# Kernel tuning notes

Hardware: AMD Instinct MI355X
Metric: run time of the kernel (lower is better)

The kernel has to match this reference:

```python
import jax, jax.numpy as jnp
import numpy as np

DIM_MODEL = 1024
N_HEAD = 16
N_HEAD_H = 16
DIM_KEY = 64
DIM_VALUE = 64


def _linear_params(key, out_f, in_f):
    kw, kb = jax.random.split(key)
    bound = 1.0 / np.sqrt(in_f)
    W = jax.random.uniform(kw, (out_f, in_f), jnp.float32, -bound, bound)
    b = jax.random.uniform(kb, (out_f,), jnp.float32, -bound, bound)
    return W, b


def setup_inputs() -> dict:
    key = jax.random.key(0)
    ks = jax.random.split(key, 12)
    B, L = 4, 1024
    queries = jax.random.normal(ks[0], (B, L, DIM_MODEL), jnp.float32)
    keys = jax.random.normal(ks[1], (B, L, DIM_MODEL), jnp.float32)
    values = jax.random.normal(ks[2], (B, L, DIM_MODEL), jnp.float32)
    mask = jnp.ones((B, L), dtype=jnp.bool_)  # accepted but unused by the module
    attn_bias = jax.random.normal(ks[3], (B, N_HEAD, L), jnp.float32)
    Wq, bq = _linear_params(ks[4], DIM_KEY * N_HEAD, DIM_MODEL)
    Wk, bk = _linear_params(ks[5], DIM_KEY * N_HEAD, DIM_MODEL)
    Wv, bv = _linear_params(ks[6], DIM_VALUE * N_HEAD, DIM_MODEL)
    Wl, bl = _linear_params(ks[7], N_HEAD_H, N_HEAD)
    Ww, bw = _linear_params(ks[8], N_HEAD, N_HEAD_H)
    Wo, bo = _linear_params(ks[9], DIM_MODEL, DIM_VALUE * N_HEAD)
    return {
        "queries": queries, "keys": keys, "values": values,
        "mask": mask, "attn_bias": attn_bias,
        "Wq": Wq, "bq": bq, "Wk": Wk, "bk": bk, "Wv": Wv, "bv": bv,
        "Wl": Wl, "bl": bl, "Ww": Ww, "bw": bw, "Wo": Wo, "bo": bo,
    }


def reference(queries, keys, values, mask, attn_bias,
              Wq, bq, Wk, bk, Wv, bv, Wl, bl, Ww, bw, Wo, bo):
    B, Lq, _ = queries.shape
    # projections -> [B, L, H, d]
    q = (queries @ Wq.T + bq).reshape(B, Lq, N_HEAD, DIM_KEY)
    k = (keys @ Wk.T + bk).reshape(B, keys.shape[1], N_HEAD, DIM_KEY)
    v = (values @ Wv.T + bv).reshape(B, values.shape[1], N_HEAD, DIM_VALUE)
    scale = DIM_KEY ** (-0.5)
    # scores in the module's [B, Lq, Lk, H] layout (after its two transposes)
    scores = jnp.einsum("bqhd,bkhd->bqkh", scale * q, k)
    # attn_bias [B, H, Lq] -> [B, Lq, 1, H], broadcast over Lk
    scores = scores + jnp.transpose(attn_bias, (0, 2, 1))[:, :, None, :]
    # pre-softmax head mixing (fc_l): [B, Lq, Lk, H] -> [B, Lq, Lk, Hh]
    logits = jnp.einsum("bqkh,gh->bqkg", scores, Wl) + bl
    weights = jax.nn.softmax(logits, axis=2)  # softmax over Lk
    # post-softmax head mixing (fc_w): [B, Lq, Lk, Hh] -> [B, Lq, Lk, H]
    weights = jnp.einsum("bqkg,hg->bqkh", weights, Ww) + bw
    # weighted values: [B, Lq, H, dv] -> combine heads -> fc_o
    ctx = jnp.einsum("bqkh,bkhd->bqhd", weights, v).reshape(B, Lq, N_HEAD * DIM_VALUE)
    return ctx @ Wo.T + bo
```

## Files before the change

### kernel.cpp

```cpp
#include <hip/hip_runtime.h>

#define L_ 1024
#define DM 1024

typedef float f32x4 __attribute__((ext_vector_type(4)));
typedef _Float16 f16;
typedef _Float16 f16x8 __attribute__((ext_vector_type(8)));
typedef _Float16 f16x4 __attribute__((ext_vector_type(4)));

__device__ __forceinline__ void gload16(const void* g, void* l) {
  __builtin_amdgcn_global_load_lds(
      (const __attribute__((address_space(1))) unsigned int*)g,
      (__attribute__((address_space(3))) unsigned int*)l, 16, 0, 0);
}

__global__ __launch_bounds__(256) void cvt_all(const float* __restrict__ q,
    const float* __restrict__ k, const float* __restrict__ v,
    const float* __restrict__ wq, const float* __restrict__ wk,
    const float* __restrict__ wv, const float* __restrict__ wo,
    f16* __restrict__ dbig, f16* __restrict__ dw, f16* __restrict__ dwo) {
  int i = blockIdx.x * 256 + threadIdx.x;
  const float* s; f16* d; int off;
  if (i < 524288)       { s = q;  d = dbig;           off = i; }
  else if (i < 1048576) { s = k;  d = dbig + 4194304; off = i - 524288; }
  else if (i < 1572864) { s = v;  d = dbig + 8388608; off = i - 1048576; }
  else if (i < 1703936) { s = wq; d = dw;             off = i - 1572864; }
  else if (i < 1835008) { s = wk; d = dw + 1048576;   off = i - 1703936; }
  else if (i < 1966080) { s = wv; d = dw + 2097152;   off = i - 1835008; }
  else                  { s = wo; d = dwo;            off = i - 1966080; }
  const float4* sp = (const float4*)s + (size_t)off * 2;
  float4 a = sp[0], bb = sp[1];
  f16x8 o;
  o[0] = (f16)a.x;  o[1] = (f16)a.y;  o[2] = (f16)a.z;  o[3] = (f16)a.w;
  o[4] = (f16)bb.x; o[5] = (f16)bb.y; o[6] = (f16)bb.z; o[7] = (f16)bb.w;
  ((f16x8*)d)[off] = o;
}

__global__ __launch_bounds__(256) void biascat(const float* __restrict__ bq,
    const float* __restrict__ bk, const float* __restrict__ bv, float* __restrict__ o) {
  int t = blockIdx.x * 256 + threadIdx.x;
  o[t] = (t < 1024) ? bq[t] : (t < 2048) ? bk[t - 1024] : bv[t - 2048];
}

__global__ __launch_bounds__(256) void proj_gemm(const f16* __restrict__ Ain,
    const f16* __restrict__ Wc, const float* __restrict__ bcat, f16* __restrict__ QKVp) {
  alignas(16) __shared__ f16 At[128 * 32];
  alignas(16) __shared__ f16 Bt[128 * 32];
  int z = blockIdx.z;
  const f16* A = Ain + (size_t)z * 4194304;
  const f16* W = Wc + (size_t)z * 1048576;
  int t = threadIdx.x, lane = t & 63;
  int w = t >> 6, wr = w >> 1, wc = w & 1;
  int bm = blockIdx.y * 128, bn = blockIdx.x * 128;
  f32x4 acc[4][4] = {};
  int rb = 32 * w + (lane >> 2);
  int c8 = (lane & 3) * 8;
  const f16* gA = A + (size_t)(bm + rb) * 1024 + c8;
  const f16* gB = W + (size_t)(bn + rb) * 1024 + c8;
  f16* lA0 = &At[(2 * w) * 512];
  f16* lA1 = &At[(2 * w + 1) * 512];
  f16* lB0 = &Bt[(2 * w) * 512];
  f16* lB1 = &Bt[(2 * w + 1) * 512];
  int ro = (lane & 15) * 32 + (lane >> 4) * 8;
  for (int kk = 0; kk < 1024; kk += 32) {
    gload16(gA + kk, lA0);
    gload16(gA + 16 * 1024 + kk, lA1);
    gload16(gB + kk, lB0);
    gload16(gB + 16 * 1024 + kk, lB1);
    __syncthreads();
    f16x8 af[4], bf[4];
    #pragma unroll
    for (int m = 0; m < 4; ++m) af[m] = *(const f16x8*)&At[(wr * 64 + m * 16) * 32 + ro];
    #pragma unroll
    for (int n = 0; n < 4; ++n) bf[n] = *(const f16x8*)&Bt[(wc * 64 + n * 16) * 32 + ro];
    #pragma unroll
    for (int m = 0; m < 4; ++m)
      #pragma unroll
      for (int n = 0; n < 4; ++n)
        acc[m][n] = __builtin_amdgcn_mfma_f32_16x16x32_f16(af[m], bf[n], acc[m][n], 0, 0, 0);
    __syncthreads();
  }
  float scale = (z == 0) ? 0.125f : 1.0f;
  #pragma unroll
  for (int n = 0; n < 4; ++n) {
    int cn = bn + wc * 64 + n * 16 + (lane & 15);
    float bvv = bcat[z * 1024 + cn];
    #pragma unroll
    for (int m = 0; m < 4; ++m) {
      int r0 = bm + wr * 64 + m * 16 + (lane >> 4) * 4;
      #pragma unroll
      for (int r = 0; r < 4; ++r)
        QKVp[(size_t)(r0 + r) * 3072 + z * 1024 + cn] = (f16)((acc[m][n][r] + bvv) * scale);
    }
  }
}

__global__ __launch_bounds__(256) void gemm_out(const f16* __restrict__ A,
    const f16* __restrict__ W, const float* __restrict__ bias, float* __restrict__ C) {
  alignas(16) __shared__ f16 At[128 * 32];
  alignas(16) __shared__ f16 Bt[128 * 32];
  int t = threadIdx.x, lane = t & 63;
  int w = t >> 6, wr = w >> 1, wc = w & 1;
  int bm = blockIdx.y * 128, bn = blockIdx.x * 128;
  f32x4 acc[4][4] = {};
  int rb = 32 * w + (lane >> 2);
  int c8 = (lane & 3) * 8;
  const f16* gA = A + (size_t)(bm + rb) * 1024 + c8;
  const f16* gB = W + (size_t)(bn + rb) * 1024 + c8;
  f16* lA0 = &At[(2 * w) * 512];
  f16* lA1 = &At[(2 * w + 1) * 512];
  f16* lB0 = &Bt[(2 * w) * 512];
  f16* lB1 = &Bt[(2 * w + 1) * 512];
  int ro = (lane & 15) * 32 + (lane >> 4) * 8;
  for (int kk = 0; kk < 1024; kk += 32) {
    gload16(gA + kk, lA0);
    gload16(gA + 16 * 1024 + kk, lA1);
    gload16(gB + kk, lB0);
    gload16(gB + 16 * 1024 + kk, lB1);
    __syncthreads();
    f16x8 af[4], bf[4];
    #pragma unroll
    for (int m = 0; m < 4; ++m) af[m] = *(const f16x8*)&At[(wr * 64 + m * 16) * 32 + ro];
    #pragma unroll
    for (int n = 0; n < 4; ++n) bf[n] = *(const f16x8*)&Bt[(wc * 64 + n * 16) * 32 + ro];
    #pragma unroll
    for (int m = 0; m < 4; ++m)
      #pragma unroll
      for (int n = 0; n < 4; ++n)
        acc[m][n] = __builtin_amdgcn_mfma_f32_16x16x32_f16(af[m], bf[n], acc[m][n], 0, 0, 0);
    __syncthreads();
  }
  #pragma unroll
  for (int n = 0; n < 4; ++n) {
    int cn = bn + wc * 64 + n * 16 + (lane & 15);
    float bvv = bias[cn];
    #pragma unroll
    for (int m = 0; m < 4; ++m) {
      int r0 = bm + wr * 64 + m * 16 + (lane >> 4) * 4;
      #pragma unroll
      for (int r = 0; r < 4; ++r)
        C[(size_t)(r0 + r) * 1024 + cn] = acc[m][n][r] + bvv;
    }
  }
}

__global__ __launch_bounds__(256) void transpose_v(const f16* __restrict__ QKVp,
                                                   f16* __restrict__ Vt) {
  alignas(16) __shared__ f16 T[64 * 72];
  int bh = blockIdx.y;
  int b = bh >> 4, h = bh & 15;
  int kt = blockIdx.x;
  int t = threadIdx.x;
  int krow = t >> 2, part = t & 3;
  const f16x8* src = (const f16x8*)(QKVp + (size_t)(b * L_ + kt * 64 + krow) * 3072 + 2048 + h * 64 + part * 16);
  f16x8 v0 = src[0], v1 = src[1];
  *(f16x8*)&T[krow * 72 + part * 16] = v0;
  *(f16x8*)&T[krow * 72 + part * 16 + 8] = v1;
  __syncthreads();
  int drow = t >> 2;
  f16x8 o0, o1;
  #pragma unroll
  for (int j = 0; j < 8; ++j) o0[j] = T[(part * 16 + j) * 72 + drow];
  #pragma unroll
  for (int j = 0; j < 8; ++j) o1[j] = T[(part * 16 + 8 + j) * 72 + drow];
  f16* dst = Vt + (size_t)(bh * 64 + drow) * L_ + kt * 64 + part * 16;
  *(f16x8*)dst = o0;
  *(f16x8*)(dst + 8) = o1;
}

__global__ __launch_bounds__(256) void cbias_kernel(const float* __restrict__ ab,
    const float* __restrict__ Wl, const float* __restrict__ bl, float* __restrict__ cb) {
  int t = blockIdx.x * 256 + threadIdx.x;
  int b = t >> 14, q = (t >> 4) & 1023, g = t & 15;
  float s = bl[g];
  #pragma unroll
  for (int h = 0; h < 16; ++h) s += ab[(size_t)(b * 16 + h) * L_ + q] * Wl[g * 16 + h];
  cb[t] = s;
}

__global__ __launch_bounds__(256) void qk_gemm(const f16* __restrict__ QKVp,
                                               f16* __restrict__ S, int b0) {
  alignas(16) __shared__ f16 At[128 * 72];
  alignas(16) __shared__ f16 Bt[128 * 72];
  int t = threadIdx.x, lane = t & 63;
  int wid = t >> 6, wr = wid >> 1, wc = wid & 1;
  int kt = blockIdx.x, qt = blockIdx.y;
  int h = blockIdx.z & 15, bz = blockIdx.z >> 4;
  int b = b0 + bz;
  #pragma unroll
  for (int i = 0; i < 4; ++i) {
    int row = i * 32 + (t >> 3), c = (t & 7) * 8;
    *(f16x8*)&At[row * 72 + c] =
        *(const f16x8*)(QKVp + (size_t)(b * 1024 + qt * 128 + row) * 3072 + h * 64 + c);
    *(f16x8*)&Bt[row * 72 + c] =
        *(const f16x8*)(QKVp + (size_t)(b * 1024 + kt * 128 + row) * 3072 + 1024 + h * 64 + c);
  }
  __syncthreads();
  int l15 = lane & 15, lhi = lane >> 4;
  f32x4 acc[4][4] = {};
  #pragma unroll
  for (int s = 0; s < 2; ++s) {
    f16x8 af[4], bf[4];
    #pragma unroll
    for (int m = 0; m < 4; ++m) af[m] = *(const f16x8*)&At[(wr * 64 + m * 16 + l15) * 72 + s * 32 + lhi * 8];
    #pragma unroll
    for (int n = 0; n < 4; ++n) bf[n] = *(const f16x8*)&Bt[(wc * 64 + n * 16 + l15) * 72 + s * 32 + lhi * 8];
    #pragma unroll
    for (int m = 0; m < 4; ++m)
      #pragma unroll
      for (int n = 0; n < 4; ++n)
        acc[m][n] = __builtin_amdgcn_mfma_f32_16x16x32_f16(af[m], bf[n], acc[m][n], 0, 0, 0);
  }
  size_t Sh = (size_t)(bz * 16 + h) * 1048576;
  #pragma unroll
  for (int n = 0; n < 4; ++n) {
    int col = kt * 128 + wc * 64 + n * 16 + l15;
    #pragma unroll
    for (int m = 0; m < 4; ++m) {
      int q0 = qt * 128 + wr * 64 + m * 16 + lhi * 4;
      #pragma unroll
      for (int r = 0; r < 4; ++r)
        S[Sh + (size_t)(q0 + r) * 1024 + col] = (f16)acc[m][n][r];
    }
  }
}

__global__ __launch_bounds__(256, 1) void msm_kernel(f16* __restrict__ S,
    const float* __restrict__ Wl, const float* __restrict__ Ww,
    const float* __restrict__ bwv, const float* __restrict__ cb, int b0) {
  alignas(16) __shared__ f16 Sl[16][1032];
  alignas(16) __shared__ f16 Sl2[1024][18];
  __shared__ float red[4][16];
  __shared__ float rlv16[16];
  int t = threadIdx.x;
  int q = blockIdx.x & 1023, bz = blockIdx.x >> 10;
  int lane = t & 63, w = t >> 6, l15 = lane & 15, lhi = lane >> 4;
  size_t Sq = (size_t)(bz * 16) * 1048576 + (size_t)q * 1024;
  #pragma unroll
  for (int i = 0; i < 8; ++i) {
    int idx = i * 256 + t, h = idx >> 7, c = (idx & 127) * 8;
    *(f16x8*)&Sl[h][c] = *(const f16x8*)(S + Sq + (size_t)h * 1048576 + c);
  }
  f16x4 b1;
  #pragma unroll
  for (int j = 0; j < 4; ++j) b1[j] = (f16)Wl[l15 * 16 + lhi * 4 + j];
  float cbv = cb[((size_t)((b0 + bz) * 1024 + q)) * 16 + l15];
  __syncthreads();
  float dsum = 0.f;
  for (int i = 0; i < 16; ++i) {
    int kt = w * 16 + i;
    int krow = kt * 16 + l15;
    f16x4 a1;
    #pragma unroll
    for (int j = 0; j < 4; ++j) a1[j] = Sl[lhi * 4 + j][krow];
    f32x4 d = __builtin_amdgcn_mfma_f32_16x16x16f16(a1, b1, (f32x4){0.f, 0.f, 0.f, 0.f}, 0, 0, 0);
    int k0 = kt * 16 + lhi * 4;
    #pragma unroll
    for (int r = 0; r < 4; ++r) {
      float e = __expf(d[r] + cbv);
      dsum += e;
      Sl2[k0 + r][l15] = (f16)e;
    }
  }
  dsum += __shfl_xor(dsum, 16);
  dsum += __shfl_xor(dsum, 32);
  if (lane < 16) red[w][lane] = dsum;
  __syncthreads();
  if (t < 16) rlv16[t] = 1.0f / (red[0][t] + red[1][t] + red[2][t] + red[3][t]);
  __syncthreads();
  f16x4 b2;
  #pragma unroll
  for (int j = 0; j < 4; ++j) b2[j] = (f16)(Ww[l15 * 16 + lhi * 4 + j] * rlv16[lhi * 4 + j]);
  float bwh = bwv[l15];
  for (int i = 0; i < 16; ++i) {
    int kt = w * 16 + i;
    int krow = kt * 16 + l15;
    f16x4 a2;
    #pragma unroll
    for (int j = 0; j < 4; ++j) a2[j] = Sl2[krow][lhi * 4 + j];
    f32x4 d = __builtin_amdgcn_mfma_f32_16x16x16f16(a2, b2, (f32x4){0.f, 0.f, 0.f, 0.f}, 0, 0, 0);
    int k0 = kt * 16 + lhi * 4;
    #pragma unroll
    for (int r = 0; r < 4; ++r) Sl[l15][k0 + r] = (f16)(d[r] + bwh);
  }
  __syncthreads();
  #pragma unroll
  for (int i = 0; i < 8; ++i) {
    int idx = i * 256 + t, h = idx >> 7, c = (idx & 127) * 8;
    *(f16x8*)(S + Sq + (size_t)h * 1048576 + c) = *(f16x8*)&Sl[h][c];
  }
}

__global__ __launch_bounds__(256) void pv_gemm(const f16* __restrict__ Sw,
    const f16* __restrict__ Vt, f16* __restrict__ ctx, int b0) {
  alignas(16) __shared__ f16 Aw[32 * 72];
  alignas(16) __shared__ f16 Bv[64 * 72];
  int t = threadIdx.x, lane = t & 63, w = t >> 6;
  int qt = blockIdx.x, h = blockIdx.y, bz = blockIdx.z;
  int wr = w >> 1, wc = w & 1;
  int l15 = lane & 15, lhi = lane >> 4;
  const f16* Sh = Sw + (size_t)(bz * 16 + h) * 1048576 + (size_t)(qt * 32) * 1024;
  const f16* Vh = Vt + (size_t)((b0 + bz) * 16 + h) * 64 * 1024;
  f32x4 acc[2] = {};
  int srow = t >> 3, scol = (t & 7) * 8;
  for (int kk = 0; kk < 1024; kk += 64) {
    __syncthreads();
    *(f16x8*)&Aw[srow * 72 + scol] = *(const f16x8*)(Sh + (size_t)srow * 1024 + kk + scol);
    *(f16x8*)&Bv[srow * 72 + scol] = *(const f16x8*)(Vh + (size_t)srow * 1024 + kk + scol);
    *(f16x8*)&Bv[(srow + 32) * 72 + scol] = *(const f16x8*)(Vh + (size_t)(srow + 32) * 1024 + kk + scol);
    __syncthreads();
    #pragma unroll
    for (int s = 0; s < 2; ++s) {
      f16x8 af = *(const f16x8*)&Aw[(wr * 16 + l15) * 72 + s * 32 + lhi * 8];
      #pragma unroll
      for (int n = 0; n < 2; ++n) {
        f16x8 bf = *(const f16x8*)&Bv[(wc * 32 + n * 16 + l15) * 72 + s * 32 + lhi * 8];
        acc[n] = __builtin_amdgcn_mfma_f32_16x16x32_f16(af, bf, acc[n], 0, 0, 0);
      }
    }
  }
  #pragma unroll
  for (int n = 0; n < 2; ++n) {
    int col = h * 64 + wc * 32 + n * 16 + l15;
    int q0 = (b0 + bz) * 1024 + qt * 32 + wr * 16 + lhi * 4;
    #pragma unroll
    for (int r = 0; r < 4; ++r)
      ctx[(size_t)(q0 + r) * 1024 + col] = (f16)acc[n][r];
  }
}

extern "C" void kernel_launch(void* const* d_in, const int* in_sizes, int n_in,
                              void* d_out, int out_size, void* d_ws, size_t ws_size,
                              hipStream_t stream) {
  const float* queries = (const float*)d_in[0];
  const float* keys    = (const float*)d_in[1];
  const float* values  = (const float*)d_in[2];
  const float* ab  = (const float*)d_in[4];
  const float* Wq  = (const float*)d_in[5];  const float* bq = (const float*)d_in[6];
  const float* Wk  = (const float*)d_in[7];  const float* bk = (const float*)d_in[8];
  const float* Wv  = (const float*)d_in[9];  const float* bv = (const float*)d_in[10];
  const float* Wl  = (const float*)d_in[11]; const float* bl = (const float*)d_in[12];
  const float* Ww  = (const float*)d_in[13]; const float* bwp = (const float*)d_in[14];
  const float* Wo  = (const float*)d_in[15]; const float* bo = (const float*)d_in[16];

  char* ws = (char*)d_ws;
  const size_t MB = 1024 * 1024;
  bool full = ws_size >= 172 * MB;

  f16* qin   = (f16*)(ws + 0 * MB);
  f16* wqkv  = (f16*)(ws + 24 * MB);
  f16* S     = (f16*)(ws + 0 * MB);
  f16* QKVp  = (f16*)(ws + (full ? 128 : 32) * MB);
  f16* Vt    = (f16*)(ws + (full ? 152 : 56) * MB);
  float* cbp = (float*)(ws + (full ? 170 : 64) * MB);
  f16* wo16  = (f16*)(ws + (full ? 168 : 65) * MB);
  f16* ctx   = (f16*)(ws + (full ? 160 : 67) * MB);
  float* bqkv = (float*)(ws + (full ? 170 * MB + 512 * 1024 : 30 * MB));

  cvt_all<<<8192, 256, 0, stream>>>(queries, keys, values, Wq, Wk, Wv, Wo, qin, wqkv, wo16);
  biascat<<<12, 256, 0, stream>>>(bq, bk, bv, bqkv);
  proj_gemm<<<dim3(8, 32, 3), 256, 0, stream>>>(qin, wqkv, bqkv, QKVp);
  transpose_v<<<dim3(16, 64), 256, 0, stream>>>(QKVp, Vt);
  cbias_kernel<<<256, 256, 0, stream>>>(ab, Wl, bl, cbp);

  if (full) {
    qk_gemm<<<dim3(8, 8, 64), 256, 0, stream>>>(QKVp, S, 0);
    msm_kernel<<<4096, 256, 0, stream>>>(S, Wl, Ww, bwp, cbp, 0);
    pv_gemm<<<dim3(32, 16, 4), 256, 0, stream>>>(S, Vt, ctx, 0);
  } else {
    for (int b = 0; b < 4; ++b) {
      qk_gemm<<<dim3(8, 8, 16), 256, 0, stream>>>(QKVp, S, b);
      msm_kernel<<<1024, 256, 0, stream>>>(S, Wl, Ww, bwp, cbp, b);
      pv_gemm<<<dim3(32, 16, 1), 256, 0, stream>>>(S, Vt, ctx, b);
    }
  }

  gemm_out<<<dim3(8, 32), 256, 0, stream>>>(ctx, wo16, bo, (float*)d_out);
}
```

Measured before the change: 213.7 us.

## Fuse QK scores with head-mixing softmax via two-pass recompute, dropping scores buffer

Replaces the separate qk_gemm and msm_kernel with a fused attn_ab kernel that computes QK scores in registers and applies the pre-softmax head mix with packed fp16 dot2. A first pass accumulates the softmax denominators per key quarter, combine_rl reduces them, and a second pass recomputes the scores, normalises, applies the post-softmax mix and writes only the final weights. This removes the write and read-back of the raw score tensor, at the cost of computing QK twice and launching only 256 blocks with heavy register use. It also drops the low-workspace fallback path and assumes the large workspace is always available.

```diff
diff --git a/kernel.cpp b/kernel.cpp
--- a/kernel.cpp
+++ b/kernel.cpp
@@ -7,12 +7,29 @@
 typedef _Float16 f16;
 typedef _Float16 f16x8 __attribute__((ext_vector_type(8)));
 typedef _Float16 f16x4 __attribute__((ext_vector_type(4)));
+typedef _Float16 f16x2 __attribute__((ext_vector_type(2)));
 
 __device__ __forceinline__ void gload16(const void* g, void* l) {
   __builtin_amdgcn_global_load_lds(
       (const __attribute__((address_space(1))) unsigned int*)g,
       (__attribute__((address_space(3))) unsigned int*)l, 16, 0, 0);
 }
+
+__device__ __forceinline__ f16x2 pkrtz(float a, float b) {
+  return __builtin_bit_cast(f16x2, __builtin_amdgcn_cvt_pkrtz(a, b));
+}
+
+#if __has_builtin(__builtin_amdgcn_fdot2)
+__device__ __forceinline__ float DOT2(f16x2 a, f16x2 b, float c) {
+  return __builtin_amdgcn_fdot2(__builtin_bit_cast(__fp16 __attribute__((ext_vector_type(2))), a),
+                                __builtin_bit_cast(__fp16 __attribute__((ext_vector_type(2))), b),
+                                c, false);
+}
+#else
+__device__ __forceinline__ float DOT2(f16x2 a, f16x2 b, float c) {
+  return fmaf((float)a[0], (float)b[0], fmaf((float)a[1], (float)b[1], c));
+}
+#endif
 
 __global__ __launch_bounds__(256) void cvt_all(const float* __restrict__ q,
     const float* __restrict__ k, const float* __restrict__ v,
@@ -178,117 +195,194 @@
   cb[t] = s;
 }
 
-__global__ __launch_bounds__(256) void qk_gemm(const f16* __restrict__ QKVp,
-                                               f16* __restrict__ S, int b0) {
-  alignas(16) __shared__ f16 At[128 * 72];
-  alignas(16) __shared__ f16 Bt[128 * 72];
-  int t = threadIdx.x, lane = t & 63;
-  int wid = t >> 6, wr = wid >> 1, wc = wid & 1;
-  int kt = blockIdx.x, qt = blockIdx.y;
-  int h = blockIdx.z & 15, bz = blockIdx.z >> 4;
-  int b = b0 + bz;
-  #pragma unroll
-  for (int i = 0; i < 4; ++i) {
-    int row = i * 32 + (t >> 3), c = (t & 7) * 8;
-    *(f16x8*)&At[row * 72 + c] =
-        *(const f16x8*)(QKVp + (size_t)(b * 1024 + qt * 128 + row) * 3072 + h * 64 + c);
-    *(f16x8*)&Bt[row * 72 + c] =
-        *(const f16x8*)(QKVp + (size_t)(b * 1024 + kt * 128 + row) * 3072 + 1024 + h * 64 + c);
-  }
-  __syncthreads();
+template <int WRITE_W>
+__global__ __launch_bounds__(256, 1) void attn_ab(const f16* __restrict__ QKVp,
+    const float* __restrict__ Wl, const float* __restrict__ Ww, const float* __restrict__ bwv,
+    const float* __restrict__ cbp, const float* __restrict__ rlp,
+    float* __restrict__ denomP, f16* __restrict__ wG) {
+  alignas(16) __shared__ f16 Kl[2][16][1032];
+  __shared__ f16x2 wlp[16][8];
+  int bid = blockIdx.x;
+  int x = bid & 7, y = bid >> 3;
+  int b = x >> 1, qt = y & 15, kq = ((x & 1) << 1) | (y >> 4);
+  int t = threadIdx.x, lane = t & 63, wv = t >> 6;
   int l15 = lane & 15, lhi = lane >> 4;
-  f32x4 acc[4][4] = {};
-  #pragma unroll
-  for (int s = 0; s < 2; ++s) {
-    f16x8 af[4], bf[4];
-    #pragma unroll
-    for (int m = 0; m < 4; ++m) af[m] = *(const f16x8*)&At[(wr * 64 + m * 16 + l15) * 72 + s * 32 + lhi * 8];
-    #pragma unroll
-    for (int n = 0; n < 4; ++n) bf[n] = *(const f16x8*)&Bt[(wc * 64 + n * 16 + l15) * 72 + s * 32 + lhi * 8];
-    #pragma unroll
-    for (int m = 0; m < 4; ++m)
-      #pragma unroll
-      for (int n = 0; n < 4; ++n)
-        acc[m][n] = __builtin_amdgcn_mfma_f32_16x16x32_f16(af[m], bf[n], acc[m][n], 0, 0, 0);
-  }
-  size_t Sh = (size_t)(bz * 16 + h) * 1048576;
-  #pragma unroll
-  for (int n = 0; n < 4; ++n) {
-    int col = kt * 128 + wc * 64 + n * 16 + l15;
-    #pragma unroll
-    for (int m = 0; m < 4; ++m) {
-      int q0 = qt * 128 + wr * 64 + m * 16 + lhi * 4;
+  if (t < 128) {
+    int g = t >> 3, p = t & 7;
+    wlp[g][p] = pkrtz(Wl[g * 16 + 2 * p], Wl[g * 16 + 2 * p + 1]);
+  }
+  int qg = b * 1024 + qt * 64 + wv * 16 + l15;
+  f16x8 qf[16][2];
+  #pragma unroll
+  for (int h = 0; h < 16; ++h)
+    #pragma unroll
+    for (int s = 0; s < 2; ++s)
+      qf[h][s] = *(const f16x8*)(QKVp + (size_t)qg * 3072 + h * 64 + s * 32 + lhi * 8);
+  float cbl[16];
+  #pragma unroll
+  for (int g4 = 0; g4 < 4; ++g4)
+    *(f32x4*)&cbl[g4 * 4] = *(const f32x4*)(cbp + (size_t)qg * 16 + g4 * 4);
+  float rlv[16];
+  float dacc[16] = {};
+  if constexpr (WRITE_W) {
+    #pragma unroll
+    for (int g4 = 0; g4 < 4; ++g4)
+      *(f32x4*)&rlv[g4 * 4] = *(const f32x4*)(rlp + (size_t)qg * 16 + g4 * 4);
+  }
+
+  auto stage = [&](int nb, int it) {
+    int k0 = b * 1024 + kq * 256 + it * 16;
+    #pragma unroll
+    for (int j = 0; j < 4; ++j) {
+      int row = wv * 4 + j;
+      const f16* src = QKVp + (size_t)(k0 + row) * 3072 + 1024 + lane * 8;
+      gload16(src, &Kl[nb][row][0]);
+      gload16(src + 512, &Kl[nb][row][512]);
+    }
+  };
+
+  if constexpr (WRITE_W) {
+    __shared__ f16x2 wwp[16][8];
+    alignas(16) __shared__ f16 WT[16][64][20];
+    if (t >= 128) {
+      int h = (t - 128) >> 3, p = (t - 128) & 7;
+      wwp[h][p] = pkrtz(Ww[h * 16 + 2 * p], Ww[h * 16 + 2 * p + 1]);
+    }
+    float bwl[16];
+    #pragma unroll
+    for (int h = 0; h < 16; ++h) bwl[h] = bwv[h];
+    stage(0, 0);
+    __syncthreads();
+    for (int it = 0; it < 16; ++it) {
+      int cur = it & 1;
+      if (it < 15) stage(cur ^ 1, it + 1);
+      f32x4 acc[16];
+      #pragma unroll
+      for (int h = 0; h < 16; ++h) {
+        f16x8 a0 = *(const f16x8*)&Kl[cur][l15][h * 64 + lhi * 8];
+        f16x8 a1 = *(const f16x8*)&Kl[cur][l15][h * 64 + 32 + lhi * 8];
+        acc[h] = __builtin_amdgcn_mfma_f32_16x16x32_f16(a0, qf[h][0], (f32x4){0.f, 0.f, 0.f, 0.f}, 0, 0, 0);
+        acc[h] = __builtin_amdgcn_mfma_f32_16x16x32_f16(a1, qf[h][1], acc[h], 0, 0, 0);
+      }
+      f16x2 sp[4][8];
+      #pragma unroll
+      for (int p = 0; p < 8; ++p)
+        #pragma unroll
+        for (int r = 0; r < 4; ++r)
+          sp[r][p] = pkrtz(acc[2 * p][r], acc[2 * p + 1][r]);
+      float E[4][16];
+      #pragma unroll
+      for (int g = 0; g < 16; ++g) {
+        f16x2 wl[8];
+        #pragma unroll
+        for (int p = 0; p < 8; ++p) wl[p] = wlp[g][p];
+        #pragma unroll
+        for (int r = 0; r < 4; ++r) {
+          float lg = cbl[g];
+          #pragma unroll
+          for (int p = 0; p < 8; ++p) lg = DOT2(sp[r][p], wl[p], lg);
+          E[r][g] = __expf(lg);
+        }
+      }
+      f16x2 pp[4][8];
       #pragma unroll
       for (int r = 0; r < 4; ++r)
-        S[Sh + (size_t)(q0 + r) * 1024 + col] = (f16)acc[m][n][r];
-    }
-  }
-}
-
-__global__ __launch_bounds__(256, 1) void msm_kernel(f16* __restrict__ S,
-    const float* __restrict__ Wl, const float* __restrict__ Ww,
-    const float* __restrict__ bwv, const float* __restrict__ cb, int b0) {
-  alignas(16) __shared__ f16 Sl[16][1032];
-  alignas(16) __shared__ f16 Sl2[1024][18];
-  __shared__ float red[4][16];
-  __shared__ float rlv16[16];
-  int t = threadIdx.x;
-  int q = blockIdx.x & 1023, bz = blockIdx.x >> 10;
-  int lane = t & 63, w = t >> 6, l15 = lane & 15, lhi = lane >> 4;
-  size_t Sq = (size_t)(bz * 16) * 1048576 + (size_t)q * 1024;
-  #pragma unroll
-  for (int i = 0; i < 8; ++i) {
-    int idx = i * 256 + t, h = idx >> 7, c = (idx & 127) * 8;
-    *(f16x8*)&Sl[h][c] = *(const f16x8*)(S + Sq + (size_t)h * 1048576 + c);
-  }
-  f16x4 b1;
-  #pragma unroll
-  for (int j = 0; j < 4; ++j) b1[j] = (f16)Wl[l15 * 16 + lhi * 4 + j];
-  float cbv = cb[((size_t)((b0 + bz) * 1024 + q)) * 16 + l15];
-  __syncthreads();
-  float dsum = 0.f;
-  for (int i = 0; i < 16; ++i) {
-    int kt = w * 16 + i;
-    int krow = kt * 16 + l15;
-    f16x4 a1;
-    #pragma unroll
-    for (int j = 0; j < 4; ++j) a1[j] = Sl[lhi * 4 + j][krow];
-    f32x4 d = __builtin_amdgcn_mfma_f32_16x16x16f16(a1, b1, (f32x4){0.f, 0.f, 0.f, 0.f}, 0, 0, 0);
-    int k0 = kt * 16 + lhi * 4;
-    #pragma unroll
-    for (int r = 0; r < 4; ++r) {
-      float e = __expf(d[r] + cbv);
-      dsum += e;
-      Sl2[k0 + r][l15] = (f16)e;
-    }
-  }
-  dsum += __shfl_xor(dsum, 16);
-  dsum += __shfl_xor(dsum, 32);
-  if (lane < 16) red[w][lane] = dsum;
-  __syncthreads();
-  if (t < 16) rlv16[t] = 1.0f / (red[0][t] + red[1][t] + red[2][t] + red[3][t]);
-  __syncthreads();
-  f16x4 b2;
-  #pragma unroll
-  for (int j = 0; j < 4; ++j) b2[j] = (f16)(Ww[l15 * 16 + lhi * 4 + j] * rlv16[lhi * 4 + j]);
-  float bwh = bwv[l15];
-  for (int i = 0; i < 16; ++i) {
-    int kt = w * 16 + i;
-    int krow = kt * 16 + l15;
-    f16x4 a2;
-    #pragma unroll
-    for (int j = 0; j < 4; ++j) a2[j] = Sl2[krow][lhi * 4 + j];
-    f32x4 d = __builtin_amdgcn_mfma_f32_16x16x16f16(a2, b2, (f32x4){0.f, 0.f, 0.f, 0.f}, 0, 0, 0);
-    int k0 = kt * 16 + lhi * 4;
-    #pragma unroll
-    for (int r = 0; r < 4; ++r) Sl[l15][k0 + r] = (f16)(d[r] + bwh);
-  }
-  __syncthreads();
-  #pragma unroll
-  for (int i = 0; i < 8; ++i) {
-    int idx = i * 256 + t, h = idx >> 7, c = (idx & 127) * 8;
-    *(f16x8*)(S + Sq + (size_t)h * 1048576 + c) = *(f16x8*)&Sl[h][c];
-  }
+        #pragma unroll
+        for (int p = 0; p < 8; ++p)
+          pp[r][p] = pkrtz(E[r][2 * p] * rlv[2 * p], E[r][2 * p + 1] * rlv[2 * p + 1]);
+      int wq = wv * 16 + l15;
+      #pragma unroll
+      for (int h = 0; h < 16; ++h) {
+        f16x2 ww[8];
+        #pragma unroll
+        for (int p = 0; p < 8; ++p) ww[p] = wwp[h][p];
+        float wr_[4];
+        #pragma unroll
+        for (int r = 0; r < 4; ++r) {
+          float a = bwl[h];
+          #pragma unroll
+          for (int p = 0; p < 8; ++p) a = DOT2(pp[r][p], ww[p], a);
+          wr_[r] = a;
+        }
+        f16x2 lo = pkrtz(wr_[0], wr_[1]);
+        f16x2 hi = pkrtz(wr_[2], wr_[3]);
+        f16x4 o; o[0] = lo[0]; o[1] = lo[1]; o[2] = hi[0]; o[3] = hi[1];
+        *(f16x4*)&WT[h][wq][lhi * 4] = o;
+      }
+      __syncthreads();
+      #pragma unroll
+      for (int i = 0; i < 4; ++i) {
+        int rid = i * 256 + t;
+        int h = rid >> 6, qq = rid & 63;
+        const f16* srcw = &WT[h][qq][0];
+        f16x4 v0 = *(const f16x4*)(srcw + 0), v1 = *(const f16x4*)(srcw + 4);
+        f16x4 v2 = *(const f16x4*)(srcw + 8), v3 = *(const f16x4*)(srcw + 12);
+        f16x8 o0, o1;
+        #pragma unroll
+        for (int j = 0; j < 4; ++j) { o0[j] = v0[j]; o0[j + 4] = v1[j]; o1[j] = v2[j]; o1[j + 4] = v3[j]; }
+        f16* dst = wG + (size_t)(b * 16 + h) * 1048576 + (size_t)(qt * 64 + qq) * 1024 + kq * 256 + it * 16;
+        *(f16x8*)dst = o0;
+        *(f16x8*)(dst + 8) = o1;
+      }
+      __syncthreads();
+    }
+  } else {
+    stage(0, 0);
+    __syncthreads();
+    for (int it = 0; it < 16; ++it) {
+      int cur = it & 1;
+      if (it < 15) stage(cur ^ 1, it + 1);
+      f32x4 acc[16];
+      #pragma unroll
+      for (int h = 0; h < 16; ++h) {
+        f16x8 a0 = *(const f16x8*)&Kl[cur][l15][h * 64 + lhi * 8];
+        f16x8 a1 = *(const f16x8*)&Kl[cur][l15][h * 64 + 32 + lhi * 8];
+        acc[h] = __builtin_amdgcn_mfma_f32_16x16x32_f16(a0, qf[h][0], (f32x4){0.f, 0.f, 0.f, 0.f}, 0, 0, 0);
+        acc[h] = __builtin_amdgcn_mfma_f32_16x16x32_f16(a1, qf[h][1], acc[h], 0, 0, 0);
+      }
+      f16x2 sp[4][8];
+      #pragma unroll
+      for (int p = 0; p < 8; ++p)
+        #pragma unroll
+        for (int r = 0; r < 4; ++r)
+          sp[r][p] = pkrtz(acc[2 * p][r], acc[2 * p + 1][r]);
+      #pragma unroll
+      for (int g = 0; g < 16; ++g) {
+        f16x2 wl[8];
+        #pragma unroll
+        for (int p = 0; p < 8; ++p) wl[p] = wlp[g][p];
+        float e0 = 0.f, e1 = 0.f;
+        #pragma unroll
+        for (int r = 0; r < 4; ++r) {
+          float lg = cbl[g];
+          #pragma unroll
+          for (int p = 0; p < 8; ++p) lg = DOT2(sp[r][p], wl[p], lg);
+          if (r & 1) e1 += __expf(lg); else e0 += __expf(lg);
+        }
+        dacc[g] += e0 + e1;
+      }
+      __syncthreads();
+    }
+    #pragma unroll
+    for (int g = 0; g < 16; ++g) {
+      float v = dacc[g];
+      v += __shfl_xor(v, 16);
+      v += __shfl_xor(v, 32);
+      dacc[g] = v;
+    }
+    if (lhi == 0) {
+      float* dst = denomP + (size_t)kq * 65536 + (size_t)qg * 16;
+      #pragma unroll
+      for (int g4 = 0; g4 < 4; ++g4)
+        *(f32x4*)(dst + g4 * 4) = *(const f32x4*)&dacc[g4 * 4];
+    }
+  }
+}
+
+__global__ __launch_bounds__(256) void combine_rl(const float* __restrict__ dp,
+                                                  float* __restrict__ rl) {
+  int i = blockIdx.x * 256 + threadIdx.x;
+  rl[i] = 1.0f / (dp[i] + dp[65536 + i] + dp[131072 + i] + dp[196608 + i]);
 }
 
 __global__ __launch_bounds__(256) void pv_gemm(const f16* __restrict__ Sw,
@@ -345,17 +439,17 @@
 
   char* ws = (char*)d_ws;
   const size_t MB = 1024 * 1024;
-  bool full = ws_size >= 172 * MB;
-
   f16* qin   = (f16*)(ws + 0 * MB);
   f16* wqkv  = (f16*)(ws + 24 * MB);
-  f16* S     = (f16*)(ws + 0 * MB);
-  f16* QKVp  = (f16*)(ws + (full ? 128 : 32) * MB);
-  f16* Vt    = (f16*)(ws + (full ? 152 : 56) * MB);
-  float* cbp = (float*)(ws + (full ? 170 : 64) * MB);
-  f16* wo16  = (f16*)(ws + (full ? 168 : 65) * MB);
-  f16* ctx   = (f16*)(ws + (full ? 160 : 67) * MB);
-  float* bqkv = (float*)(ws + (full ? 170 * MB + 512 * 1024 : 30 * MB));
+  f16* wG    = (f16*)(ws + 0 * MB);
+  f16* QKVp  = (f16*)(ws + 128 * MB);
+  f16* Vt    = (f16*)(ws + 152 * MB);
+  f16* ctx   = (f16*)(ws + 160 * MB);
+  f16* wo16  = (f16*)(ws + 168 * MB);
+  float* cbp = (float*)(ws + 170 * MB);
+  float* rlp = (float*)(ws + 170 * MB + 256 * 1024);
+  float* dnp = (float*)(ws + 170 * MB + 512 * 1024);
+  float* bqkv = (float*)(ws + 171 * MB + 512 * 1024);
 
   cvt_all<<<8192, 256, 0, stream>>>(queries, keys, values, Wq, Wk, Wv, Wo, qin, wqkv, wo16);
   biascat<<<12, 256, 0, stream>>>(bq, bk, bv, bqkv);
@@ -363,17 +457,10 @@
   transpose_v<<<dim3(16, 64), 256, 0, stream>>>(QKVp, Vt);
   cbias_kernel<<<256, 256, 0, stream>>>(ab, Wl, bl, cbp);
 
-  if (full) {
-    qk_gemm<<<dim3(8, 8, 64), 256, 0, stream>>>(QKVp, S, 0);
-    msm_kernel<<<4096, 256, 0, stream>>>(S, Wl, Ww, bwp, cbp, 0);
-    pv_gemm<<<dim3(32, 16, 4), 256, 0, stream>>>(S, Vt, ctx, 0);
-  } else {
-    for (int b = 0; b < 4; ++b) {
-      qk_gemm<<<dim3(8, 8, 16), 256, 0, stream>>>(QKVp, S, b);
-      msm_kernel<<<1024, 256, 0, stream>>>(S, Wl, Ww, bwp, cbp, b);
-      pv_gemm<<<dim3(32, 16, 1), 256, 0, stream>>>(S, Vt, ctx, b);
-    }
-  }
-
+  attn_ab<0><<<256, 256, 0, stream>>>(QKVp, Wl, Ww, bwp, cbp, rlp, dnp, wG);
+  combine_rl<<<256, 256, 0, stream>>>(dnp, rlp);
+  attn_ab<1><<<256, 256, 0, stream>>>(QKVp, Wl, Ww, bwp, cbp, rlp, dnp, wG);
+
+  pv_gemm<<<dim3(32, 16, 4), 256, 0, stream>>>(wG, Vt, ctx, 0);
   gemm_out<<<dim3(8, 32), 256, 0, stream>>>(ctx, wo16, bo, (float*)d_out);
 }
```

New measurement: 307.1 us. +43.7%, slower.

## Fuse QK, head-mixing softmax and PV into two-pass flash-style attention kernel

Applied to the files above, without the earlier changes.

Replaces the materialized score tensor (qk_gemm, msm_kernel, pv_gemm over a B*H*L*L fp16 buffer) with a fused kernel run twice. The first pass computes softmax denominators and the second recomputes the scores and accumulates the context, with the key dimension split in two halves whose partial results are combined afterwards. The post-softmax bias term is folded out algebraically using precomputed column sums of V. This removes the large global-memory round trips of the score matrix, at the cost of computing QK twice and running small grids (512 blocks, one block per CU) with scattered global K/V loads issued directly from each wave without LDS staging.

```diff
diff --git a/kernel.cpp b/kernel.cpp
--- a/kernel.cpp
+++ b/kernel.cpp
@@ -168,6 +168,25 @@
   *(f16x8*)(dst + 8) = o1;
 }
 
+__global__ __launch_bounds__(256) void vcolsum(const f16* __restrict__ Vt,
+                                               float* __restrict__ Vcs) {
+  __shared__ float red[256];
+  int bh = blockIdx.x;
+  int t = threadIdx.x;
+  int d = t & 63, part = t >> 6;
+  const f16x8* row = (const f16x8*)(Vt + (size_t)(bh * 64 + d) * 1024 + part * 256);
+  float s = 0.f;
+  #pragma unroll
+  for (int i = 0; i < 32; ++i) {
+    f16x8 v = row[i];
+    #pragma unroll
+    for (int j = 0; j < 8; ++j) s += (float)v[j];
+  }
+  red[part * 64 + d] = s;
+  __syncthreads();
+  if (t < 64) Vcs[bh * 64 + t] = red[t] + red[64 + t] + red[128 + t] + red[192 + t];
+}
+
 __global__ __launch_bounds__(256) void cbias_kernel(const float* __restrict__ ab,
     const float* __restrict__ Wl, const float* __restrict__ bl, float* __restrict__ cb) {
   int t = blockIdx.x * 256 + threadIdx.x;
@@ -178,155 +197,156 @@
   cb[t] = s;
 }
 
-__global__ __launch_bounds__(256) void qk_gemm(const f16* __restrict__ QKVp,
-                                               f16* __restrict__ S, int b0) {
-  alignas(16) __shared__ f16 At[128 * 72];
-  alignas(16) __shared__ f16 Bt[128 * 72];
-  int t = threadIdx.x, lane = t & 63;
-  int wid = t >> 6, wr = wid >> 1, wc = wid & 1;
-  int kt = blockIdx.x, qt = blockIdx.y;
-  int h = blockIdx.z & 15, bz = blockIdx.z >> 4;
-  int b = b0 + bz;
-  #pragma unroll
-  for (int i = 0; i < 4; ++i) {
-    int row = i * 32 + (t >> 3), c = (t & 7) * 8;
-    *(f16x8*)&At[row * 72 + c] =
-        *(const f16x8*)(QKVp + (size_t)(b * 1024 + qt * 128 + row) * 3072 + h * 64 + c);
-    *(f16x8*)&Bt[row * 72 + c] =
-        *(const f16x8*)(QKVp + (size_t)(b * 1024 + kt * 128 + row) * 3072 + 1024 + h * 64 + c);
-  }
-  __syncthreads();
+template <int PASS>
+__global__ __launch_bounds__(256, 1) void attn_fused(const f16* __restrict__ QKVp,
+    const f16* __restrict__ Vt, const float* __restrict__ Wl, const float* __restrict__ Ww,
+    const float* __restrict__ cbp, const float* __restrict__ rlp,
+    float* __restrict__ dnp, float* __restrict__ dctx) {
+  alignas(16) __shared__ f16 Sx[32][17][18];
+  alignas(16) __shared__ f16 Wx[16][17][40];
+  __shared__ float red[4][16][16];
+  int bid = blockIdx.x;
+  int x = bid & 7, rr = bid >> 3;
+  int b = x >> 1;
+  int sub = ((x & 1) << 6) + rr;
+  int qt = sub & 63, kq = sub >> 6;
+  int t = threadIdx.x, lane = t & 63, wv = t >> 6;
   int l15 = lane & 15, lhi = lane >> 4;
-  f32x4 acc[4][4] = {};
-  #pragma unroll
-  for (int s = 0; s < 2; ++s) {
-    f16x8 af[4], bf[4];
-    #pragma unroll
-    for (int m = 0; m < 4; ++m) af[m] = *(const f16x8*)&At[(wr * 64 + m * 16 + l15) * 72 + s * 32 + lhi * 8];
-    #pragma unroll
-    for (int n = 0; n < 4; ++n) bf[n] = *(const f16x8*)&Bt[(wc * 64 + n * 16 + l15) * 72 + s * 32 + lhi * 8];
-    #pragma unroll
-    for (int m = 0; m < 4; ++m)
-      #pragma unroll
-      for (int n = 0; n < 4; ++n)
-        acc[m][n] = __builtin_amdgcn_mfma_f32_16x16x32_f16(af[m], bf[n], acc[m][n], 0, 0, 0);
-  }
-  size_t Sh = (size_t)(bz * 16 + h) * 1048576;
-  #pragma unroll
-  for (int n = 0; n < 4; ++n) {
-    int col = kt * 128 + wc * 64 + n * 16 + l15;
-    #pragma unroll
-    for (int m = 0; m < 4; ++m) {
-      int q0 = qt * 128 + wr * 64 + m * 16 + lhi * 4;
-      #pragma unroll
-      for (int r = 0; r < 4; ++r)
-        S[Sh + (size_t)(q0 + r) * 1024 + col] = (f16)acc[m][n][r];
-    }
-  }
-}
-
-__global__ __launch_bounds__(256, 1) void msm_kernel(f16* __restrict__ S,
-    const float* __restrict__ Wl, const float* __restrict__ Ww,
-    const float* __restrict__ bwv, const float* __restrict__ cb, int b0) {
-  alignas(16) __shared__ f16 Sl[16][1032];
-  alignas(16) __shared__ f16 Sl2[1024][18];
-  __shared__ float red[4][16];
-  __shared__ float rlv16[16];
-  int t = threadIdx.x;
-  int q = blockIdx.x & 1023, bz = blockIdx.x >> 10;
-  int lane = t & 63, w = t >> 6, l15 = lane & 15, lhi = lane >> 4;
-  size_t Sq = (size_t)(bz * 16) * 1048576 + (size_t)q * 1024;
-  #pragma unroll
-  for (int i = 0; i < 8; ++i) {
-    int idx = i * 256 + t, h = idx >> 7, c = (idx & 127) * 8;
-    *(f16x8*)&Sl[h][c] = *(const f16x8*)(S + Sq + (size_t)h * 1048576 + c);
-  }
-  f16x4 b1;
-  #pragma unroll
-  for (int j = 0; j < 4; ++j) b1[j] = (f16)Wl[l15 * 16 + lhi * 4 + j];
-  float cbv = cb[((size_t)((b0 + bz) * 1024 + q)) * 16 + l15];
-  __syncthreads();
-  float dsum = 0.f;
-  for (int i = 0; i < 16; ++i) {
-    int kt = w * 16 + i;
-    int krow = kt * 16 + l15;
-    f16x4 a1;
-    #pragma unroll
-    for (int j = 0; j < 4; ++j) a1[j] = Sl[lhi * 4 + j][krow];
-    f32x4 d = __builtin_amdgcn_mfma_f32_16x16x16f16(a1, b1, (f32x4){0.f, 0.f, 0.f, 0.f}, 0, 0, 0);
-    int k0 = kt * 16 + lhi * 4;
-    #pragma unroll
-    for (int r = 0; r < 4; ++r) {
-      float e = __expf(d[r] + cbv);
-      dsum += e;
-      Sl2[k0 + r][l15] = (f16)e;
-    }
-  }
-  dsum += __shfl_xor(dsum, 16);
-  dsum += __shfl_xor(dsum, 32);
-  if (lane < 16) red[w][lane] = dsum;
-  __syncthreads();
-  if (t < 16) rlv16[t] = 1.0f / (red[0][t] + red[1][t] + red[2][t] + red[3][t]);
-  __syncthreads();
-  f16x4 b2;
-  #pragma unroll
-  for (int j = 0; j < 4; ++j) b2[j] = (f16)(Ww[l15 * 16 + lhi * 4 + j] * rlv16[lhi * 4 + j]);
-  float bwh = bwv[l15];
-  for (int i = 0; i < 16; ++i) {
-    int kt = w * 16 + i;
-    int krow = kt * 16 + l15;
-    f16x4 a2;
-    #pragma unroll
-    for (int j = 0; j < 4; ++j) a2[j] = Sl2[krow][lhi * 4 + j];
-    f32x4 d = __builtin_amdgcn_mfma_f32_16x16x16f16(a2, b2, (f32x4){0.f, 0.f, 0.f, 0.f}, 0, 0, 0);
-    int k0 = kt * 16 + lhi * 4;
-    #pragma unroll
-    for (int r = 0; r < 4; ++r) Sl[l15][k0 + r] = (f16)(d[r] + bwh);
-  }
-  __syncthreads();
-  #pragma unroll
-  for (int i = 0; i < 8; ++i) {
-    int idx = i * 256 + t, h = idx >> 7, c = (idx & 127) * 8;
-    *(f16x8*)(S + Sq + (size_t)h * 1048576 + c) = *(f16x8*)&Sl[h][c];
-  }
-}
-
-__global__ __launch_bounds__(256) void pv_gemm(const f16* __restrict__ Sw,
-    const f16* __restrict__ Vt, f16* __restrict__ ctx, int b0) {
-  alignas(16) __shared__ f16 Aw[32 * 72];
-  alignas(16) __shared__ f16 Bv[64 * 72];
-  int t = threadIdx.x, lane = t & 63, w = t >> 6;
-  int qt = blockIdx.x, h = blockIdx.y, bz = blockIdx.z;
-  int wr = w >> 1, wc = w & 1;
-  int l15 = lane & 15, lhi = lane >> 4;
-  const f16* Sh = Sw + (size_t)(bz * 16 + h) * 1048576 + (size_t)(qt * 32) * 1024;
-  const f16* Vh = Vt + (size_t)((b0 + bz) * 16 + h) * 64 * 1024;
-  f32x4 acc[2] = {};
-  int srow = t >> 3, scol = (t & 7) * 8;
-  for (int kk = 0; kk < 1024; kk += 64) {
-    __syncthreads();
-    *(f16x8*)&Aw[srow * 72 + scol] = *(const f16x8*)(Sh + (size_t)srow * 1024 + kk + scol);
-    *(f16x8*)&Bv[srow * 72 + scol] = *(const f16x8*)(Vh + (size_t)srow * 1024 + kk + scol);
-    *(f16x8*)&Bv[(srow + 32) * 72 + scol] = *(const f16x8*)(Vh + (size_t)(srow + 32) * 1024 + kk + scol);
-    __syncthreads();
-    #pragma unroll
-    for (int s = 0; s < 2; ++s) {
-      f16x8 af = *(const f16x8*)&Aw[(wr * 16 + l15) * 72 + s * 32 + lhi * 8];
-      #pragma unroll
-      for (int n = 0; n < 2; ++n) {
-        f16x8 bf = *(const f16x8*)&Bv[(wc * 32 + n * 16 + l15) * 72 + s * 32 + lhi * 8];
-        acc[n] = __builtin_amdgcn_mfma_f32_16x16x32_f16(af, bf, acc[n], 0, 0, 0);
+  f16x4 wlB, wwB;
+  #pragma unroll
+  for (int j = 0; j < 4; ++j) {
+    wlB[j] = (f16)Wl[l15 * 16 + lhi * 4 + j];
+    wwB[j] = (f16)Ww[l15 * 16 + lhi * 4 + j];
+  }
+  f16x8 qfr[4][2];
+  #pragma unroll
+  for (int hh = 0; hh < 4; ++hh)
+    #pragma unroll
+    for (int s = 0; s < 2; ++s)
+      qfr[hh][s] = *(const f16x8*)(QKVp + (size_t)(b * 1024 + qt * 16 + l15) * 3072
+                                   + (wv * 4 + hh) * 64 + s * 32 + lhi * 8);
+  float cb4[4], rl4[4];
+  #pragma unroll
+  for (int r = 0; r < 4; ++r)
+    cb4[r] = cbp[(size_t)((b << 10) + qt * 16 + lhi * 4 + r) * 16 + l15];
+  if constexpr (PASS == 1) {
+    #pragma unroll
+    for (int r = 0; r < 4; ++r)
+      rl4[r] = rlp[(size_t)((b << 10) + qt * 16 + lhi * 4 + r) * 16 + l15];
+  }
+  float dacc[4] = {};
+  f32x4 ctx[4][4] = {};
+  f16* wxp = &Wx[0][0][0];
+
+  for (int tile = 0; tile < 16; ++tile) {
+    int k0 = b * 1024 + kq * 512 + tile * 32;
+    #pragma unroll
+    for (int kt2 = 0; kt2 < 2; ++kt2) {
+      f32x4 sa[4];
+      #pragma unroll
+      for (int hh = 0; hh < 4; ++hh) {
+        int h = wv * 4 + hh;
+        const f16* kp = QKVp + (size_t)(k0 + kt2 * 16 + l15) * 3072 + 1024 + h * 64 + lhi * 8;
+        f16x8 a0 = *(const f16x8*)kp;
+        f16x8 a1 = *(const f16x8*)(kp + 32);
+        f32x4 a = __builtin_amdgcn_mfma_f32_16x16x32_f16(a0, qfr[hh][0], (f32x4){0.f, 0.f, 0.f, 0.f}, 0, 0, 0);
+        sa[hh] = __builtin_amdgcn_mfma_f32_16x16x32_f16(a1, qfr[hh][1], a, 0, 0, 0);
       }
-    }
-  }
-  #pragma unroll
-  for (int n = 0; n < 2; ++n) {
-    int col = h * 64 + wc * 32 + n * 16 + l15;
-    int q0 = (b0 + bz) * 1024 + qt * 32 + wr * 16 + lhi * 4;
-    #pragma unroll
-    for (int r = 0; r < 4; ++r)
-      ctx[(size_t)(q0 + r) * 1024 + col] = (f16)acc[n][r];
-  }
+      #pragma unroll
+      for (int r = 0; r < 4; ++r) {
+        f16x4 v;
+        v[0] = (f16)sa[0][r]; v[1] = (f16)sa[1][r];
+        v[2] = (f16)sa[2][r]; v[3] = (f16)sa[3][r];
+        *(f16x4*)&Sx[kt2 * 16 + lhi * 4 + r][l15][wv * 4] = v;
+      }
+    }
+    __syncthreads();
+    #pragma unroll
+    for (int i = 0; i < 8; ++i) {
+      int kk = wv * 8 + i;
+      f16x4 a1 = *(const f16x4*)&Sx[kk][l15][lhi * 4];
+      f32x4 Lg = __builtin_amdgcn_mfma_f32_16x16x16f16(a1, wlB, (f32x4){0.f, 0.f, 0.f, 0.f}, 0, 0, 0);
+      if constexpr (PASS == 0) {
+        #pragma unroll
+        for (int r = 0; r < 4; ++r) dacc[r] += __expf(Lg[r] + cb4[r]);
+      } else {
+        #pragma unroll
+        for (int r = 0; r < 4; ++r) {
+          float p = __expf(Lg[r] + cb4[r]) * rl4[r];
+          Sx[kk][lhi * 4 + r][l15] = (f16)p;
+        }
+        f16x4 a2 = *(const f16x4*)&Sx[kk][l15][lhi * 4];
+        f32x4 W2 = __builtin_amdgcn_mfma_f32_16x16x16f16(a2, wwB, (f32x4){0.f, 0.f, 0.f, 0.f}, 0, 0, 0);
+        #pragma unroll
+        for (int r = 0; r < 4; ++r)
+          wxp[(lhi * 4 + r) * 680 + l15 * 40 + kk] = (f16)W2[r];
+      }
+    }
+    if constexpr (PASS == 1) {
+      __syncthreads();
+      #pragma unroll
+      for (int hh = 0; hh < 4; ++hh) {
+        int h = wv * 4 + hh;
+        f16x8 aw = *(const f16x8*)&wxp[l15 * 680 + h * 40 + lhi * 8];
+        #pragma unroll
+        for (int dn = 0; dn < 4; ++dn) {
+          f16x8 bv = *(const f16x8*)(Vt + (size_t)((b * 16 + h) * 64 + dn * 16 + l15) * 1024
+                                     + kq * 512 + tile * 32 + lhi * 8);
+          ctx[hh][dn] = __builtin_amdgcn_mfma_f32_16x16x32_f16(aw, bv, ctx[hh][dn], 0, 0, 0);
+        }
+      }
+    }
+    __syncthreads();
+  }
+  if constexpr (PASS == 0) {
+    #pragma unroll
+    for (int r = 0; r < 4; ++r) red[wv][lhi * 4 + r][l15] = dacc[r];
+    __syncthreads();
+    int q = t >> 4, g = t & 15;
+    float s = red[0][q][g] + red[1][q][g] + red[2][q][g] + red[3][q][g];
+    dnp[(size_t)kq * 65536 + (size_t)((b << 10) + qt * 16 + q) * 16 + g] = s;
+  } else {
+    float* dst = dctx + (size_t)kq * 4194304;
+    #pragma unroll
+    for (int hh = 0; hh < 4; ++hh) {
+      int h = wv * 4 + hh;
+      #pragma unroll
+      for (int dn = 0; dn < 4; ++dn)
+        #pragma unroll
+        for (int r = 0; r < 4; ++r)
+          dst[(size_t)((b << 10) + qt * 16 + lhi * 4 + r) * 1024 + h * 64 + dn * 16 + l15] = ctx[hh][dn][r];
+    }
+  }
+}
+
+__global__ __launch_bounds__(256) void combine_rl(const float* __restrict__ dp,
+                                                  float* __restrict__ rl) {
+  int i = blockIdx.x * 256 + threadIdx.x;
+  rl[i] = 1.0f / (dp[i] + dp[65536 + i]);
+}
+
+__global__ __launch_bounds__(256) void ctx_final(const float* __restrict__ d0,
+    const float* __restrict__ d1, const float* __restrict__ Vcs,
+    const float* __restrict__ bwv, f16* __restrict__ ctx) {
+  int e = blockIdx.x * 256 + threadIdx.x;
+  size_t base = (size_t)e * 8;
+  int c = (int)(base & 1023);
+  int brow = (int)(base >> 10);
+  int b = brow >> 10;
+  float bwh = bwv[c >> 6];
+  const float4* p0 = (const float4*)(d0 + base);
+  const float4* p1 = (const float4*)(d1 + base);
+  const float4* pv = (const float4*)(Vcs + b * 1024 + c);
+  f16x8 o;
+  #pragma unroll
+  for (int half = 0; half < 2; ++half) {
+    float4 a = p0[half], bb = p1[half], vv = pv[half];
+    o[half * 4 + 0] = (f16)(a.x + bb.x + bwh * vv.x);
+    o[half * 4 + 1] = (f16)(a.y + bb.y + bwh * vv.y);
+    o[half * 4 + 2] = (f16)(a.z + bb.z + bwh * vv.z);
+    o[half * 4 + 3] = (f16)(a.w + bb.w + bwh * vv.w);
+  }
+  ((f16x8*)ctx)[e] = o;
 }
 
 extern "C" void kernel_launch(void* const* d_in, const int* in_sizes, int n_in,
@@ -345,35 +365,30 @@
 
   char* ws = (char*)d_ws;
   const size_t MB = 1024 * 1024;
-  bool full = ws_size >= 172 * MB;
-
   f16* qin   = (f16*)(ws + 0 * MB);
   f16* wqkv  = (f16*)(ws + 24 * MB);
-  f16* S     = (f16*)(ws + 0 * MB);
-  f16* QKVp  = (f16*)(ws + (full ? 128 : 32) * MB);
-  f16* Vt    = (f16*)(ws + (full ? 152 : 56) * MB);
-  float* cbp = (float*)(ws + (full ? 170 : 64) * MB);
-  f16* wo16  = (f16*)(ws + (full ? 168 : 65) * MB);
-  f16* ctx   = (f16*)(ws + (full ? 160 : 67) * MB);
-  float* bqkv = (float*)(ws + (full ? 170 * MB + 512 * 1024 : 30 * MB));
+  float* dctx = (float*)(ws + 0 * MB);
+  f16* QKVp  = (f16*)(ws + 32 * MB);
+  f16* Vt    = (f16*)(ws + 56 * MB);
+  f16* ctx   = (f16*)(ws + 64 * MB);
+  f16* wo16  = (f16*)(ws + 72 * MB);
+  float* cbp = (float*)(ws + 74 * MB);
+  float* rlp = (float*)(ws + 74 * MB + 256 * 1024);
+  float* dnp = (float*)(ws + 74 * MB + 512 * 1024);
+  float* vcs = (float*)(ws + 75 * MB);
+  float* bqkv = (float*)(ws + 75 * MB + 64 * 1024);
 
   cvt_all<<<8192, 256, 0, stream>>>(queries, keys, values, Wq, Wk, Wv, Wo, qin, wqkv, wo16);
   biascat<<<12, 256, 0, stream>>>(bq, bk, bv, bqkv);
   proj_gemm<<<dim3(8, 32, 3), 256, 0, stream>>>(qin, wqkv, bqkv, QKVp);
   transpose_v<<<dim3(16, 64), 256, 0, stream>>>(QKVp, Vt);
+  vcolsum<<<64, 256, 0, stream>>>(Vt, vcs);
   cbias_kernel<<<256, 256, 0, stream>>>(ab, Wl, bl, cbp);
 
-  if (full) {
-    qk_gemm<<<dim3(8, 8, 64), 256, 0, stream>>>(QKVp, S, 0);
-    msm_kernel<<<4096, 256, 0, stream>>>(S, Wl, Ww, bwp, cbp, 0);
-    pv_gemm<<<dim3(32, 16, 4), 256, 0, stream>>>(S, Vt, ctx, 0);
-  } else {
-    for (int b = 0; b < 4; ++b) {
-      qk_gemm<<<dim3(8, 8, 16), 256, 0, stream>>>(QKVp, S, b);
-      msm_kernel<<<1024, 256, 0, stream>>>(S, Wl, Ww, bwp, cbp, b);
-      pv_gemm<<<dim3(32, 16, 1), 256, 0, stream>>>(S, Vt, ctx, b);
-    }
-  }
+  attn_fused<0><<<512, 256, 0, stream>>>(QKVp, Vt, Wl, Ww, cbp, rlp, dnp, dctx);
+  combine_rl<<<256, 256, 0, stream>>>(dnp, rlp);
+  attn_fused<1><<<512, 256, 0, stream>>>(QKVp, Vt, Wl, Ww, cbp, rlp, dnp, dctx);
+  ctx_final<<<2048, 256, 0, stream>>>(dctx, dctx + 4194304, vcs, bwp, ctx);
 
   gemm_out<<<dim3(8, 32), 256, 0, stream>>>(ctx, wo16, bo, (float*)d_out);
 }
```

Result: slower. 356.7 us (+66.9%).
